# Optimization experiments

Hardware: AMD Instinct MI355X
Metric: run time of the kernel (lower is better)

The kernel has to match this reference:

```python
import jax, jax.numpy as jnp
import numpy as np

INIT_STD = 0.002
DEFAULT_BETA = 1.0 / np.sqrt(64.0)  # 1/sqrt(head_dim)


def setup_inputs() -> dict:
    key = jax.random.key(0)
    k1, k2, k3 = jax.random.split(key, 3)
    B, S, E = 4, 2048, 768
    H, D = 12, 64
    x = jax.random.normal(k1, (B, S, E), dtype=jnp.float32)
    q_proj_weight = INIT_STD * jax.random.normal(k2, (H, D, E), dtype=jnp.float32)
    k_proj_weight = INIT_STD * jax.random.normal(k3, (H, D, E), dtype=jnp.float32)
    beta = jnp.full((H,), DEFAULT_BETA, dtype=jnp.float32)
    return {"x": x, "q_proj_weight": q_proj_weight, "k_proj_weight": k_proj_weight, "beta": beta}


def reference(x, q_proj_weight, k_proj_weight, beta):
    # x: [B,S,E]; W^{Q,K}: [H,D,E]; beta: [H]
    q = jnp.einsum("bse,hde->bshd", x, q_proj_weight)  # [B,S,H,D]
    k = jnp.einsum("bse,hde->bshd", x, k_proj_weight)  # [B,S,H,D]
    # scores[b,h,s,t] = beta_h * <Q_{bsh}, K_{bth}>
    scores = jnp.einsum("bshd,bthd,h->bhst", q, k, beta)
    S = x.shape[1]
    diag = jnp.eye(S, dtype=bool)  # self-exclusion mask (B != C)
    scores = jnp.where(diag[None, None, :, :], -jnp.inf, scores)
    lse = jax.nn.logsumexp(scores, axis=-1)  # [B,H,S]
    # E = -sum_{b,h,s} (1/beta_h) * logsumexp_t
    energy = -jnp.sum(lse / beta[None, :, None])
    return energy
```

## Files before the change

kernel.cpp:

```cpp
#include <hip/hip_runtime.h>
#include <hip/hip_bf16.h>

typedef __attribute__((ext_vector_type(8))) short short8v;
typedef __attribute__((ext_vector_type(4))) float f32x4;

static constexpr int B_ = 4, S_ = 2048, E_ = 768, H_ = 12, D_ = 64;
static constexpr int NROWS = B_ * H_ * S_;
static constexpr float LOG2E = 1.44269504088896340736f;
static constexpr float LN2 = 0.69314718055994530942f;

typedef __attribute__((address_space(3))) unsigned int lds_u32;
typedef const __attribute__((address_space(1))) unsigned int glb_u32;

__device__ __forceinline__ void gload16(const void* g, void* l) {
  __builtin_amdgcn_global_load_lds((glb_u32*)g, (lds_u32*)l, 16, 0, 0);
}

#define VM0 asm volatile("s_waitcnt vmcnt(0)" ::: "memory")
#define VM2 asm volatile("s_waitcnt vmcnt(2)" ::: "memory")
#define BAR __builtin_amdgcn_s_barrier()

__device__ __forceinline__ unsigned short f2bf(float f) {
  union { float f; unsigned int u; } v; v.f = f;
  unsigned int u = v.u;
  unsigned int r = (u + 0x7fffu + ((u >> 16) & 1u)) >> 16;
  return (unsigned short)r;
}

__global__ __launch_bounds__(256) void cvt_x_kernel(const float4* __restrict__ x,
                                                    ushort4* __restrict__ xb, int n4) {
  int i = blockIdx.x * 256 + threadIdx.x;
  if (i >= n4) return;
  float4 v = x[i];
  ushort4 o;
  o.x = f2bf(v.x); o.y = f2bf(v.y); o.z = f2bf(v.z); o.w = f2bf(v.w);
  xb[i] = o;
}

__global__ __launch_bounds__(256) void cvt_w_kernel(const float4* __restrict__ wq,
                                                    const float4* __restrict__ wk,
                                                    const float* __restrict__ beta,
                                                    ushort4* __restrict__ wb, int n4) {
  int i = blockIdx.x * 256 + threadIdx.x;
  if (i < n4) {
    int row = i / (E_ / 4);
    float sc = beta[row >> 6] * LOG2E;
    float4 v = wq[i];
    ushort4 o;
    o.x = f2bf(v.x * sc); o.y = f2bf(v.y * sc); o.z = f2bf(v.z * sc); o.w = f2bf(v.w * sc);
    wb[i] = o;
  } else if (i < 2 * n4) {
    int j = i - n4;
    float4 v = wk[j];
    ushort4 o;
    o.x = f2bf(v.x); o.y = f2bf(v.y); o.z = f2bf(v.z); o.w = f2bf(v.w);
    wb[i] = o;
  }
}

__global__ __launch_bounds__(256) void proj_kernel(const unsigned short* __restrict__ xb,
                                                   const unsigned short* __restrict__ wb,
                                                   unsigned short* __restrict__ Qb,
                                                   unsigned short* __restrict__ Kb) {
  __shared__ unsigned short lA[128 * 32];
  __shared__ unsigned short lB[128 * 32];
  const int mt = blockIdx.x, nt = blockIdx.y;
  const int t = threadIdx.x;
  const int wid = t >> 6, lane = t & 63, l15 = lane & 15, lhi = lane >> 4;
  const int wr = (wid >> 1) * 64, wc = (wid & 1) * 64;

  f32x4 acc[4][4] = {};

  const int row = t >> 2, ch = t & 3;
  const unsigned short* gA = xb + (size_t)(mt * 128 + row) * E_ + ch * 8;
  const unsigned short* gB = wb + (size_t)(nt * 128 + row) * E_ + ch * 8;

  for (int k0 = 0; k0 < E_; k0 += 32) {
    gload16(gA + k0, &lA[t * 8]);
    gload16(gA + (size_t)64 * E_ + k0, &lA[2048 + t * 8]);
    gload16(gB + k0, &lB[t * 8]);
    gload16(gB + (size_t)64 * E_ + k0, &lB[2048 + t * 8]);
    __syncthreads();
    short8v aF[4], bF[4];
#pragma unroll
    for (int m = 0; m < 4; ++m)
      aF[m] = *(const short8v*)&lA[(wr + m * 16 + l15) * 32 + lhi * 8];
#pragma unroll
    for (int n = 0; n < 4; ++n)
      bF[n] = *(const short8v*)&lB[(wc + n * 16 + l15) * 32 + lhi * 8];
#pragma unroll
    for (int m = 0; m < 4; ++m)
#pragma unroll
      for (int n = 0; n < 4; ++n)
        acc[m][n] = __builtin_amdgcn_mfma_f32_16x16x32_bf16(aF[m], bF[n], acc[m][n], 0, 0, 0);
    __syncthreads();
  }

  const int nbase = nt * 128 + wc;
  unsigned short* dst = (nbase < 768) ? Qb : Kb;
  const int nb = (nbase < 768) ? nbase : nbase - 768;
#pragma unroll
  for (int m = 0; m < 4; ++m)
#pragma unroll
    for (int n = 0; n < 4; ++n)
#pragma unroll
      for (int r = 0; r < 4; ++r) {
        int M = mt * 128 + wr + m * 16 + lhi * 4 + r;
        int col = nb + n * 16 + l15;
        int h = col >> 6, d = col & 63;
        int b = M >> 11, s = M & (S_ - 1);
        dst[((((size_t)b * H_ + h) * S_ + s) << 6) + d] = f2bf(acc[m][n][r]);
      }
}

__device__ __forceinline__ void stageK(const unsigned short* __restrict__ Kbase, int t0,
                                       int tid, unsigned short* lbuf) {
  const int w = tid >> 6;
  const int r = tid >> 3;
  const int c = (tid & 7) ^ (r & 7);
  const char* src = (const char*)Kbase + ((size_t)(t0 + r) << 7) + (c << 4);
  char* ldst = (char*)lbuf + (w << 10);
  gload16(src, ldst);
  gload16(src + (32 << 7), ldst + 4096);
}

__device__ __forceinline__ void computeTile64(const unsigned short* lbuf, const short8v q[4][2],
                                              float sp[4][4], int l15, int lhi) {
  short8v kf[4][2];
  const int sw = l15 & 7;
#pragma unroll
  for (int f = 0; f < 4; ++f) {
    const char* p = (const char*)lbuf + ((f * 16 + l15) << 7);
    kf[f][0] = *(const short8v*)(p + ((lhi ^ sw) << 4));
    kf[f][1] = *(const short8v*)(p + (((lhi + 4) ^ sw) << 4));
  }
#pragma unroll
  for (int rb = 0; rb < 4; ++rb) {
    f32x4 acc[4] = {};
#pragma unroll
    for (int f = 0; f < 4; ++f) {
      acc[f] = __builtin_amdgcn_mfma_f32_16x16x32_bf16(q[rb][0], kf[f][0], acc[f], 0, 0, 0);
      acc[f] = __builtin_amdgcn_mfma_f32_16x16x32_bf16(q[rb][1], kf[f][1], acc[f], 0, 0, 0);
    }
#pragma unroll
    for (int f = 0; f < 4; ++f)
#pragma unroll
      for (int r = 0; r < 4; ++r)
        sp[rb][r] += __builtin_amdgcn_exp2f(acc[f][r]);
  }
}

__device__ __forceinline__ void loadK(const unsigned short* __restrict__ Kbase, int t0,
                                      int l15, int lhi, short8v kf[4][2]) {
#pragma unroll
  for (int f = 0; f < 4; ++f) {
    const unsigned short* krow = Kbase + (size_t)(t0 + f * 16 + l15) * D_ + lhi * 8;
    kf[f][0] = *(const short8v*)krow;
    kf[f][1] = *(const short8v*)(krow + 32);
  }
}

__global__ __launch_bounds__(256) void lse_kernel(const unsigned short* __restrict__ Qb,
                                                  const unsigned short* __restrict__ Kb,
                                                  float* __restrict__ rowsum) {
  __shared__ __align__(16) unsigned short lK[3][4096];
  const int L = blockIdx.x + 8 * (blockIdx.y + 12 * blockIdx.z);
  const int xcd = L & 7, j = L >> 3;
  const int split = j & 3;
  const int st = (j >> 2) & 7;
  const int g = xcd + 8 * (j >> 5);
  const int h = g % H_, b = g / H_;

  const int tid = threadIdx.x;
  const int wid = tid >> 6, lane = tid & 63;
  const int l15 = lane & 15, lhi = lane >> 4;
  const size_t hb = ((size_t)b * H_ + h) * S_;
  const unsigned short* Qbase = Qb + hb * D_;
  const unsigned short* Kbase = Kb + hb * D_;
  const int s0 = st * 256 + wid * 64;
  const int tb = split * 512;

  short8v q[4][2];
#pragma unroll
  for (int rb = 0; rb < 4; ++rb) {
    const unsigned short* qr = Qbase + (size_t)(s0 + rb * 16 + l15) * D_ + lhi * 8;
    q[rb][0] = *(const short8v*)qr;
    q[rb][1] = *(const short8v*)(qr + 32);
  }

  float sp[4][4] = {};
  stageK(Kbase, tb, tid, lK[0]);
  stageK(Kbase, tb + 64, tid, lK[1]);
  int bi = 0;
#pragma unroll 1
  for (int i = 0; i < 7; ++i) {
    VM2;
    BAR;
    if (i < 6) {
      int bs_ = bi + 2; if (bs_ >= 3) bs_ -= 3;
      stageK(Kbase, tb + (i + 2) * 64, tid, lK[bs_]);
    }
    computeTile64(lK[bi], q, sp, l15, lhi);
    if (++bi == 3) bi = 0;
  }
  VM0; BAR;
  computeTile64(lK[bi], q, sp, l15, lhi);

  if ((s0 >> 9) == split) {
    short8v kD[4][2];
    loadK(Kbase, s0, l15, lhi, kD);
#pragma unroll
    for (int rb = 0; rb < 4; ++rb) {
      f32x4 acc[4] = {};
#pragma unroll
      for (int f = 0; f < 4; ++f) {
        acc[f] = __builtin_amdgcn_mfma_f32_16x16x32_bf16(q[rb][0], kD[f][0], acc[f], 0, 0, 0);
        acc[f] = __builtin_amdgcn_mfma_f32_16x16x32_bf16(q[rb][1], kD[f][1], acc[f], 0, 0, 0);
      }
#pragma unroll
      for (int f = 0; f < 4; ++f)
#pragma unroll
        for (int r = 0; r < 4; ++r) {
          int lrow = rb * 16 + lhi * 4 + r;
          int lcol = f * 16 + l15;
          if (lrow == lcol) sp[rb][r] -= __builtin_amdgcn_exp2f(acc[f][r]);
        }
    }
  }

#pragma unroll
  for (int rb = 0; rb < 4; ++rb)
#pragma unroll
    for (int r = 0; r < 4; ++r) {
      float s = sp[rb][r];
#pragma unroll
      for (int off = 1; off < 16; off <<= 1) s += __shfl_xor(s, off, 64);
      if (l15 == 0)
        rowsum[(size_t)split * NROWS + hb + s0 + rb * 16 + lhi * 4 + r] = s;
    }
}

__global__ __launch_bounds__(256) void finish1_kernel(const float* __restrict__ rowsum,
                                                      const float* __restrict__ beta,
                                                      float* __restrict__ partial) {
  int row = blockIdx.x * 256 + threadIdx.x;
  float s = (rowsum[row] + rowsum[NROWS + row]) +
            (rowsum[2 * NROWS + row] + rowsum[3 * NROWS + row]);
  int h = (row >> 11) % H_;
  float c = __builtin_amdgcn_logf(s) * LN2 / beta[h];
#pragma unroll
  for (int off = 1; off < 64; off <<= 1) c += __shfl_xor(c, off, 64);
  __shared__ float wsum[4];
  int wid = threadIdx.x >> 6;
  if ((threadIdx.x & 63) == 0) wsum[wid] = c;
  __syncthreads();
  if (threadIdx.x == 0) partial[blockIdx.x] = wsum[0] + wsum[1] + wsum[2] + wsum[3];
}

__global__ __launch_bounds__(256) void finish2_kernel(const float* __restrict__ partial, int n,
                                                      float* __restrict__ out) {
  float s = 0.f;
  for (int i = threadIdx.x; i < n; i += 256) s += partial[i];
#pragma unroll
  for (int off = 1; off < 64; off <<= 1) s += __shfl_xor(s, off, 64);
  __shared__ float wsum[4];
  int wid = threadIdx.x >> 6;
  if ((threadIdx.x & 63) == 0) wsum[wid] = s;
  __syncthreads();
  if (threadIdx.x == 0) out[0] = -(wsum[0] + wsum[1] + wsum[2] + wsum[3]);
}

extern "C" void kernel_launch(void* const* d_in, const int* in_sizes, int n_in,
                              void* d_out, int out_size, void* d_ws, size_t ws_size,
                              hipStream_t stream) {
  const float* x    = (const float*)d_in[0];
  const float* wq   = (const float*)d_in[1];
  const float* wk   = (const float*)d_in[2];
  const float* beta = (const float*)d_in[3];

  char* ws = (char*)d_ws;
  const size_t xb_bytes = (size_t)B_ * S_ * E_ * 2;
  const size_t wb_bytes = (size_t)2 * H_ * D_ * E_ * 2;
  const size_t qk_bytes = (size_t)B_ * H_ * S_ * D_ * 2;
  const size_t rs_bytes = (size_t)4 * NROWS * 4;
  unsigned short* xb = (unsigned short*)ws;
  unsigned short* wb = (unsigned short*)(ws + xb_bytes);
  unsigned short* Qb = (unsigned short*)(ws + xb_bytes + wb_bytes);
  unsigned short* Kb = (unsigned short*)(ws + xb_bytes + wb_bytes + qk_bytes);
  float* rowsum      = (float*)(ws + xb_bytes + wb_bytes + 2 * qk_bytes);
  float* partial     = (float*)(ws + xb_bytes + wb_bytes + 2 * qk_bytes + rs_bytes);

  int nx4 = (B_ * S_ * E_) / 4;
  cvt_x_kernel<<<(nx4 + 255) / 256, 256, 0, stream>>>((const float4*)x, (ushort4*)xb, nx4);

  int nw4 = (H_ * D_ * E_) / 4;
  cvt_w_kernel<<<(2 * nw4 + 255) / 256, 256, 0, stream>>>((const float4*)wq, (const float4*)wk,
                                                          beta, (ushort4*)wb, nw4);

  dim3 pgrid((B_ * S_) / 128, (2 * H_ * D_) / 128);
  proj_kernel<<<pgrid, 256, 0, stream>>>(xb, wb, Qb, Kb);

  dim3 lgrid(S_ / 256, H_, B_ * 4);
  lse_kernel<<<lgrid, 256, 0, stream>>>(Qb, Kb, rowsum);

  finish1_kernel<<<NROWS / 256, 256, 0, stream>>>(rowsum, beta, partial);
  finish2_kernel<<<1, 256, 0, stream>>>(partial, NROWS / 256, (float*)d_out);
}
```

Measured before the change: 79.33 us.

## Load K fragments directly from global memory instead of LDS staging

Replaces the triple-buffered LDS staging of K tiles (global_load_lds plus barriers) with per-wave direct global loads of K fragments into registers. The diagonal self-exclusion is folded into the main loop by zeroing the exp on the diagonal tile, which removes the extra K reload and MFMA pass. It also raises wave priority around the MFMA block with s_setprio. This drops barrier and LDS traffic, but each wave now loads K itself and relies on L2/cache hits, and load latency is no longer hidden by explicit prefetch.

```diff
diff --git a/kernel.cpp b/kernel.cpp
--- a/kernel.cpp
+++ b/kernel.cpp
@@ -15,10 +15,6 @@
 __device__ __forceinline__ void gload16(const void* g, void* l) {
   __builtin_amdgcn_global_load_lds((glb_u32*)g, (lds_u32*)l, 16, 0, 0);
 }
-
-#define VM0 asm volatile("s_waitcnt vmcnt(0)" ::: "memory")
-#define VM2 asm volatile("s_waitcnt vmcnt(2)" ::: "memory")
-#define BAR __builtin_amdgcn_s_barrier()
 
 __device__ __forceinline__ unsigned short f2bf(float f) {
   union { float f; unsigned int u; } v; v.f = f;
@@ -113,57 +109,9 @@
       }
 }
 
-__device__ __forceinline__ void stageK(const unsigned short* __restrict__ Kbase, int t0,
-                                       int tid, unsigned short* lbuf) {
-  const int w = tid >> 6;
-  const int r = tid >> 3;
-  const int c = (tid & 7) ^ (r & 7);
-  const char* src = (const char*)Kbase + ((size_t)(t0 + r) << 7) + (c << 4);
-  char* ldst = (char*)lbuf + (w << 10);
-  gload16(src, ldst);
-  gload16(src + (32 << 7), ldst + 4096);
-}
-
-__device__ __forceinline__ void computeTile64(const unsigned short* lbuf, const short8v q[4][2],
-                                              float sp[4][4], int l15, int lhi) {
-  short8v kf[4][2];
-  const int sw = l15 & 7;
-#pragma unroll
-  for (int f = 0; f < 4; ++f) {
-    const char* p = (const char*)lbuf + ((f * 16 + l15) << 7);
-    kf[f][0] = *(const short8v*)(p + ((lhi ^ sw) << 4));
-    kf[f][1] = *(const short8v*)(p + (((lhi + 4) ^ sw) << 4));
-  }
-#pragma unroll
-  for (int rb = 0; rb < 4; ++rb) {
-    f32x4 acc[4] = {};
-#pragma unroll
-    for (int f = 0; f < 4; ++f) {
-      acc[f] = __builtin_amdgcn_mfma_f32_16x16x32_bf16(q[rb][0], kf[f][0], acc[f], 0, 0, 0);
-      acc[f] = __builtin_amdgcn_mfma_f32_16x16x32_bf16(q[rb][1], kf[f][1], acc[f], 0, 0, 0);
-    }
-#pragma unroll
-    for (int f = 0; f < 4; ++f)
-#pragma unroll
-      for (int r = 0; r < 4; ++r)
-        sp[rb][r] += __builtin_amdgcn_exp2f(acc[f][r]);
-  }
-}
-
-__device__ __forceinline__ void loadK(const unsigned short* __restrict__ Kbase, int t0,
-                                      int l15, int lhi, short8v kf[4][2]) {
-#pragma unroll
-  for (int f = 0; f < 4; ++f) {
-    const unsigned short* krow = Kbase + (size_t)(t0 + f * 16 + l15) * D_ + lhi * 8;
-    kf[f][0] = *(const short8v*)krow;
-    kf[f][1] = *(const short8v*)(krow + 32);
-  }
-}
-
 __global__ __launch_bounds__(256) void lse_kernel(const unsigned short* __restrict__ Qb,
                                                   const unsigned short* __restrict__ Kb,
                                                   float* __restrict__ rowsum) {
-  __shared__ __align__(16) unsigned short lK[3][4096];
   const int L = blockIdx.x + 8 * (blockIdx.y + 12 * blockIdx.z);
   const int xcd = L & 7, j = L >> 3;
   const int split = j & 3;
@@ -188,43 +136,45 @@
     q[rb][1] = *(const short8v*)(qr + 32);
   }
 
-  float sp[4][4] = {};
-  stageK(Kbase, tb, tid, lK[0]);
-  stageK(Kbase, tb + 64, tid, lK[1]);
-  int bi = 0;
+  const int dtile = ((s0 >> 9) == split) ? ((s0 - tb) >> 6) : -1;
+
+  f32x4 sp[4] = {};
+  const unsigned short* kp = Kbase + ((size_t)tb << 6);
+
 #pragma unroll 1
-  for (int i = 0; i < 7; ++i) {
-    VM2;
-    BAR;
-    if (i < 6) {
-      int bs_ = bi + 2; if (bs_ >= 3) bs_ -= 3;
-      stageK(Kbase, tb + (i + 2) * 64, tid, lK[bs_]);
+  for (int i = 0; i < 8; ++i) {
+    short8v kf[4][2];
+#pragma unroll
+    for (int f = 0; f < 4; ++f) {
+      const unsigned short* kr = kp + ((f * 16 + l15) << 6) + lhi * 8;
+      kf[f][0] = *(const short8v*)kr;
+      kf[f][1] = *(const short8v*)(kr + 32);
     }
-    computeTile64(lK[bi], q, sp, l15, lhi);
-    if (++bi == 3) bi = 0;
-  }
-  VM0; BAR;
-  computeTile64(lK[bi], q, sp, l15, lhi);
-
-  if ((s0 >> 9) == split) {
-    short8v kD[4][2];
-    loadK(Kbase, s0, l15, lhi, kD);
+    kp += 64 * D_;
+    const bool isD = (i == dtile);
+
 #pragma unroll
     for (int rb = 0; rb < 4; ++rb) {
       f32x4 acc[4] = {};
+      __builtin_amdgcn_s_setprio(1);
 #pragma unroll
       for (int f = 0; f < 4; ++f) {
-        acc[f] = __builtin_amdgcn_mfma_f32_16x16x32_bf16(q[rb][0], kD[f][0], acc[f], 0, 0, 0);
-        acc[f] = __builtin_amdgcn_mfma_f32_16x16x32_bf16(q[rb][1], kD[f][1], acc[f], 0, 0, 0);
+        acc[f] = __builtin_amdgcn_mfma_f32_16x16x32_bf16(q[rb][0], kf[f][0], acc[f], 0, 0, 0);
+        acc[f] = __builtin_amdgcn_mfma_f32_16x16x32_bf16(q[rb][1], kf[f][1], acc[f], 0, 0, 0);
       }
-#pragma unroll
-      for (int f = 0; f < 4; ++f)
-#pragma unroll
-        for (int r = 0; r < 4; ++r) {
-          int lrow = rb * 16 + lhi * 4 + r;
-          int lcol = f * 16 + l15;
-          if (lrow == lcol) sp[rb][r] -= __builtin_amdgcn_exp2f(acc[f][r]);
+      __builtin_amdgcn_s_setprio(0);
+#pragma unroll
+      for (int f = 0; f < 4; ++f) {
+        f32x4 e;
+#pragma unroll
+        for (int r = 0; r < 4; ++r) e[r] = __builtin_amdgcn_exp2f(acc[f][r]);
+        if (f == rb && isD) {
+#pragma unroll
+          for (int r = 0; r < 4; ++r)
+            if (l15 == lhi * 4 + r) e[r] = 0.f;
         }
+        sp[rb] += e;
+      }
     }
   }
 
```

New measurement: 96.32 us. +21.4%, slower.
